# Performance work log

Hardware: AMD Instinct MI355X
Metric: run time of the kernel (lower is better)

## Reference

```python
import jax, jax.numpy as jnp
import numpy as np

B, D, C_IN = 2, 64, 4
N1, N2, N3, N4 = 32, 64, 96, 128
MQ, K = 1024, 5
DN = ('NCDHW', 'OIDHW', 'NCDHW')
PAD = [(2, 2)] * 3  # centered 5^3 kernel, matches Minkowski offsets in [-2, 2]


def setup_inputs() -> dict:
    rng = np.random.default_rng(0)
    mask = rng.random((B, D, D, D)) < 0.2
    x_feat = (rng.standard_normal((B, C_IN, D, D, D)) * mask[:, None]).astype(np.float32)
    Q_F = rng.random((B, MQ, 2)).astype(np.float32)  # per-point quality features (2 channels)

    def conv(cin, cout):
        w = (rng.standard_normal((cout, cin, K, K, K)) / np.sqrt(cin * K ** 3)).astype(np.float32)
        b = (0.01 * rng.standard_normal(cout)).astype(np.float32)
        return w, b

    def gdn(c):
        beta = np.ones(c, np.float32)
        gamma = (1e-4 * rng.random((c, c, K, K, K))).astype(np.float32)
        gamma[np.arange(c), np.arange(c), K // 2, K // 2, K // 2] += 0.1
        return beta, gamma

    w1, b1 = conv(C_IN, N1)
    w2, b2 = conv(N1, N2)
    w3, b3 = conv(N2, N3)
    w4, b4 = conv(N3, N4)
    beta1, gamma1 = gdn(N1)
    beta2, gamma2 = gdn(N2)
    beta3, gamma3 = gdn(N3)
    out = dict(x_feat=x_feat, mask=mask, Q_F=Q_F,
               w1=w1, b1=b1, w2=w2, b2=b2, w3=w3, b3=b3, w4=w4, b4=b4,
               beta1=beta1, gamma1=gamma1, beta2=beta2, gamma2=gamma2,
               beta3=beta3, gamma3=gamma3)
    return {k: jnp.asarray(v) for k, v in out.items()}


def _conv3d(x, w, b, stride):
    y = jax.lax.conv_general_dilated(x, w, (stride,) * 3, PAD, dimension_numbers=DN)
    return y + b[None, :, None, None, None]


def _pool_mask(m):
    # Minkowski stride-2 output coords = any occupied input in each 2x2x2 cell
    b, d = m.shape[0], m.shape[1]
    return m.reshape(b, d // 2, 2, d // 2, 2, d // 2, 2).max(axis=(2, 4, 6))


def _gdn(x, beta, gamma, scale, m):
    # conditional GDN: y = x / sqrt(beta + conv5(gamma, x^2)), scaled per batch by q[:,0]
    den = jax.lax.conv_general_dilated(x * x, gamma, (1, 1, 1), PAD, dimension_numbers=DN)
    y = x * jax.lax.rsqrt(beta[None, :, None, None, None] + den)
    return y * scale * m[:, None]


def reference(x_feat, mask, Q_F, w1, b1, w2, b2, w3, b3, w4, b4,
              beta1, gamma1, beta2, gamma2, beta3, gamma3):
    m0 = mask.astype(x_feat.dtype)
    q = jnp.mean(Q_F, axis=1)[None]                       # [1, B, 2]: per-batch mean of Q.F
    scale = q[0, :, 0][:, None, None, None, None]         # per-batch conditional scale

    c0 = m0.sum(axis=(1, 2, 3))                           # count_per_batch(x)
    m1 = _pool_mask(m0)
    x = _gdn(_conv3d(x_feat, w1, b1, 2) * m1[:, None], beta1, gamma1, scale, m1)
    c1 = m1.sum(axis=(1, 2, 3))
    m2 = _pool_mask(m1)
    x = _gdn(_conv3d(x, w2, b2, 2) * m2[:, None], beta2, gamma2, scale, m2)
    c2 = m2.sum(axis=(1, 2, 3))
    m3 = _pool_mask(m2)
    x = _gdn(_conv3d(x, w3, b3, 2) * m3[:, None], beta3, gamma3, scale, m3)
    x = _conv3d(x, w4, b4, 1) * m3[:, None]               # stride-1 conv keeps coords
    k = jnp.stack([c2, c1, c0]).astype(jnp.int32)         # k.reverse() in the original
    return x, q, k
```

## Files before the change

### kernel.cpp

```cpp
#include <hip/hip_runtime.h>
#include <math.h>

constexpr int Bn  = 2;
constexpr int CIN = 4;
constexpr int MQn = 1024;
constexpr int D0 = 64, D1 = 32, D2 = 16, D3 = 8;

constexpr int OUT_X = 0;
constexpr int OUT_Q = 131072;
constexpr int OUT_K = 131076;

constexpr size_t OFF_CNT   = 0;
constexpr size_t OFF_ZERO  = 8;
constexpr size_t OFF_D1    = 16;
constexpr size_t OFF_T2    = OFF_D1 + 2097152;
constexpr size_t OFF_D2    = OFF_T2 + 524288;
constexpr size_t OFF_T3    = OFF_D2 + 524288;
constexpr size_t OFF_D3    = OFF_T3 + 98304;
constexpr size_t ZERO_END  = OFF_D3 + 98304;
constexpr size_t OFF_SCALE = 3342360;
constexpr size_t OFF_M1    = 3342368;
constexpr size_t OFF_M2    = OFF_M1 + 65536;
constexpr size_t OFF_M3    = OFF_M2 + 8192;
constexpr size_t OFF_T1    = OFF_M3 + 1024;
constexpr size_t OFF_Y1    = OFF_T1 + 2097152;
constexpr size_t OFF_Y2    = OFF_Y1 + 2097152;
constexpr size_t OFF_SQ1   = OFF_Y2 + 524288;
constexpr size_t OFF_SQ2   = OFF_SQ1 + 1048576;
constexpr size_t OFF_SQ3   = OFF_SQ2 + 262144;
constexpr size_t OFF_Y3C   = OFF_SQ3 + 49152;
constexpr size_t OFF_W1T   = OFF_Y3C + 49152;
constexpr size_t OFF_W2T   = OFF_W1T + 16000;
constexpr size_t OFF_W3T   = OFF_W2T + 256000;
constexpr size_t OFF_WB1   = OFF_W3T + 768000;
constexpr size_t OFF_WB2   = OFF_WB1 + 64000;
constexpr size_t OFF_WB3   = OFF_WB2 + 256000;
constexpr size_t OFF_WB4   = OFF_WB3 + 576000;
constexpr size_t OFF_PU    = 12248736;
constexpr size_t OFF_Y1P   = OFF_PU + 9437184;
constexpr size_t OFF_WB2S  = OFF_Y1P + 3145728;
constexpr size_t OFF_WB1S  = OFF_WB2S + 384000;
constexpr size_t OFF_WB3S  = OFF_WB1S + 32000;
constexpr size_t OFF_Y2HL  = OFF_WB3S + 1152000;

typedef float v4f __attribute__((ext_vector_type(4)));
typedef __attribute__((ext_vector_type(8)))  short bf16x8v;
typedef __attribute__((ext_vector_type(4)))  short bf16x4v;
typedef __attribute__((ext_vector_type(16))) float f32x16v;

__device__ __forceinline__ void async_copy16(const float* g, float* l) {
    __builtin_amdgcn_global_load_lds(
        (const __attribute__((address_space(1))) void*)g,
        (__attribute__((address_space(3))) void*)l, 16, 0, 0);
}
__device__ __forceinline__ unsigned short f2bf(float f) {
    unsigned u = __float_as_uint(f);
    return (unsigned short)((u + 0x7FFFu + ((u >> 16) & 1u)) >> 16);
}
__device__ __forceinline__ float bf2f(unsigned short h) {
    return __uint_as_float((unsigned)h << 16);
}

__global__ void qmean_kernel(const float* __restrict__ QF, float* __restrict__ out_q,
                             float* __restrict__ scale) {
    int b = blockIdx.x >> 1, c = blockIdx.x & 1;
    float s = 0.f;
    for (int m = threadIdx.x; m < MQn; m += blockDim.x)
        s += QF[(b * MQn + m) * 2 + c];
    __shared__ float sh[256];
    sh[threadIdx.x] = s;
    __syncthreads();
    for (int st = 128; st > 0; st >>= 1) {
        if (threadIdx.x < st) sh[threadIdx.x] += sh[threadIdx.x + st];
        __syncthreads();
    }
    if (threadIdx.x == 0) {
        float mean = sh[0] / (float)MQn;
        out_q[b * 2 + c] = mean;
        if (c == 0) scale[b] = mean;
    }
}

__global__ void mask_pool1_kernel(const float* __restrict__ xf, float* __restrict__ m1,
                                  float* __restrict__ c0) {
    int idx = blockIdx.x * blockDim.x + threadIdx.x;
    int b = idx >> 15;
    int v = idx & 32767;
    int oz = v >> 10, oy = (v >> 5) & 31, ox = v & 31;
    float cnt = 0.f, mx = 0.f;
    for (int dz = 0; dz < 2; ++dz)
        for (int dy = 0; dy < 2; ++dy)
            for (int dx = 0; dx < 2; ++dx) {
                int z = 2 * oz + dz, y = 2 * oy + dy, x = 2 * ox + dx;
                size_t base = (size_t)b * CIN * D0 * D0 * D0 + ((size_t)z * D0 + y) * D0 + x;
                bool occ = false;
                for (int c = 0; c < CIN; ++c)
                    occ = occ || (xf[base + (size_t)c * D0 * D0 * D0] != 0.f);
                if (occ) { cnt += 1.f; mx = 1.f; }
            }
    m1[idx] = mx;
    __shared__ float sh[256];
    sh[threadIdx.x] = cnt;
    __syncthreads();
    for (int st = 128; st > 0; st >>= 1) {
        if (threadIdx.x < st) sh[threadIdx.x] += sh[threadIdx.x + st];
        __syncthreads();
    }
    if (threadIdx.x == 0) atomicAdd(&c0[b], sh[0]);
}

__global__ void pool_kernel(const float* __restrict__ min_, float* __restrict__ mout,
                            float* __restrict__ cacc, int Din) {
    int Do = Din >> 1;
    int per = Do * Do * Do;
    int idx = blockIdx.x * blockDim.x + threadIdx.x;
    int b = idx / per;
    int v = idx % per;
    int oz = v / (Do * Do), oy = (v / Do) % Do, ox = v % Do;
    float s = 0.f, mx = 0.f;
    for (int dz = 0; dz < 2; ++dz)
        for (int dy = 0; dy < 2; ++dy)
            for (int dx = 0; dx < 2; ++dx) {
                float val = min_[(((size_t)b * Din + 2 * oz + dz) * Din + 2 * oy + dy) * Din + 2 * ox + dx];
                s += val;
                mx = fmaxf(mx, val);
            }
    mout[idx] = mx;
    __shared__ float sh[256];
    sh[threadIdx.x] = s;
    __syncthreads();
    for (int st = 128; st > 0; st >>= 1) {
        if (threadIdx.x < st) sh[threadIdx.x] += sh[threadIdx.x + st];
        __syncthreads();
    }
    if (threadIdx.x == 0) atomicAdd(&cacc[b], sh[0]);
}

__global__ void writek_kernel(const float* __restrict__ cnt, float* __restrict__ outk) {
    int i = threadIdx.x;
    if (i < 6) {
        int row = i >> 1, b = i & 1;
        float v = (row == 0) ? cnt[4 + b] : (row == 1 ? cnt[2 + b] : cnt[b]);
        outk[i] = v;
    }
}

constexpr int MS1 = 0,        ME1 = 128000;
constexpr int MS2 = 128000,   ME2 = 640000;
constexpr int MS3 = 640000,   ME3 = 1792000;
constexpr int MS4 = 1792000,  ME4 = 3328000;
__global__ __launch_bounds__(256) void mwtrans_all_kernel(
        const float* __restrict__ g1, const float* __restrict__ g2,
        const float* __restrict__ g3, const float* __restrict__ w4,
        float* __restrict__ ws) {
    int idx = blockIdx.x * 256 + threadIdx.x;
    if (idx >= ME4) return;
    const float* src; unsigned short* dst; int nchn, cin, o;
    if (idx < ME1)      { src = g1; dst = (unsigned short*)(ws + OFF_WB1); nchn = 1; cin = 32; o = idx - MS1; }
    else if (idx < ME2) { src = g2; dst = (unsigned short*)(ws + OFF_WB2); nchn = 2; cin = 64; o = idx - MS2; }
    else if (idx < ME3) { src = g3; dst = (unsigned short*)(ws + OFF_WB3); nchn = 3; cin = 96; o = idx - MS3; }
    else                { src = w4; dst = (unsigned short*)(ws + OFF_WB4); nchn = 4; cin = 96; o = idx - MS4; }
    int j  = o & 7;
    int kc = (o >> 3) & 1;
    int n  = (o >> 4) & 31;
    int q  = o >> 9;
    int tap = q % 125;
    int q2  = q / 125;
    int nch = q2 % nchn;
    int cs  = q2 / nchn;
    int co = nch * 32 + n;
    int ci = cs * 16 + kc * 8 + j;
    dst[o] = f2bf(src[((size_t)co * cin + ci) * 125 + tap]);
}

constexpr int W2S_N = 768000;
__global__ __launch_bounds__(256) void w2s_kernel(const float* __restrict__ w2,
        unsigned short* __restrict__ dst) {
    int o = blockIdx.x * 256 + threadIdx.x;
    if (o >= W2S_N) return;
    int j = o & 7; int kc = (o >> 3) & 1; int n = (o >> 4) & 31; int q = o >> 9;
    int tap = q % 125; int q2 = q / 125; int c = q2 & 1; int cs = q2 >> 1;
    int co = c * 32 + n;
    int e = cs * 16 + kc * 8 + j;
    int ci = e & 31;
    float wv = w2[((size_t)co * 32 + ci) * 125 + tap];
    unsigned short h = f2bf(wv);
    if (e >= 64) h = f2bf(wv - bf2f(h));
    dst[o] = h;
}

constexpr int W3S_N = 2304000;
__global__ __launch_bounds__(256) void w3s_kernel(const float* __restrict__ w3,
        unsigned short* __restrict__ dst) {
    int o = blockIdx.x * 256 + threadIdx.x;
    if (o >= W3S_N) return;
    int j = o & 7; int kc = (o >> 3) & 1; int n = (o >> 4) & 31; int q = o >> 9;
    int tap = q % 125; int q2 = q / 125; int nch = q2 % 3; int cs = q2 / 3;
    int co = nch * 32 + n;
    int e = cs * 16 + kc * 8 + j;
    int ci = e & 63;
    float wv = w3[((size_t)co * 64 + ci) * 125 + tap];
    unsigned short h = f2bf(wv);
    if (e >= 128) h = f2bf(wv - bf2f(h));
    dst[o] = h;
}

constexpr int W1S_N = 64000;
__global__ __launch_bounds__(256) void w1s_kernel(const float* __restrict__ w1,
        unsigned short* __restrict__ dst) {
    int o = blockIdx.x * 256 + threadIdx.x;
    if (o >= W1S_N) return;
    int j = o & 7; int kc = (o >> 3) & 1; int n = (o >> 4) & 31; int tap = o >> 9;
    int ci = j & 3;
    unsigned short h;
    float wv = w1[((size_t)n * 4 + ci) * 125 + tap];
    unsigned short hi = f2bf(wv);
    if (kc == 0)       h = hi;
    else if (j < 4)    h = f2bf(wv - bf2f(hi));
    else               h = 0;
    dst[o] = h;
}

__global__ __launch_bounds__(256) void xcl_kernel(const float* __restrict__ xf,
        unsigned short* __restrict__ xcl) {
    int idx = blockIdx.x * 256 + threadIdx.x;
    int s = idx & 262143; int b = idx >> 18;
    bf16x8v o;
#pragma unroll
    for (int ci = 0; ci < 4; ++ci) {
        float f = xf[((size_t)(b * 4 + ci) << 18) + s];
        unsigned short h = f2bf(f);
        o[ci] = (short)h;
        o[4 + ci] = (short)f2bf(f - bf2f(h));
    }
    *(bf16x8v*)(xcl + (size_t)idx * 8) = o;
}

__global__ __launch_bounds__(256) void mconv1_s2_kernel(
    const unsigned short* __restrict__ xcl,
    const unsigned short* __restrict__ wb,
    const float* __restrict__ bias, const float* __restrict__ mask,
    const float* __restrict__ zerow,
    float* __restrict__ t1, unsigned short* __restrict__ sqcl)
{
    constexpr int DIN = 64, DOUT = 32;
    constexpr int NTX = 4, NTY = 8;
    int r = blockIdx.x;
    int tx0 = (r % NTX) * 8; r /= NTX;
    int ty0 = (r % NTY) * 4; r /= NTY;
    int tz0 = (r % 8) * 4;   int b = r / 8;

    int tid = threadIdx.x;
    int lane = tid & 63, w = tid >> 6;
    int n = lane & 31, kc = lane >> 5;
    int oz = tz0 + w, oy = ty0 + (n >> 3), ox = tx0 + (n & 7);

    f32x16v acc;
#pragma unroll
    for (int i = 0; i < 16; ++i) acc[i] = 0.f;

#pragma unroll 1
    for (int kz = 0; kz < 5; ++kz) {
        int gz = 2 * oz + kz - 2;
        bool zok = (unsigned)gz < (unsigned)DIN;
#pragma unroll 1
        for (int ky = 0; ky < 5; ++ky) {
            int gy = 2 * oy + ky - 2;
            bool zyok = zok && ((unsigned)gy < (unsigned)DIN);
            long long rowbase = (((long long)(b * DIN + gz) * DIN + gy) * DIN) * 8;
#pragma unroll
            for (int kx = 0; kx < 5; ++kx) {
                int gx = 2 * ox + kx - 2;
                bool ok = zyok && ((unsigned)gx < (unsigned)DIN);
                const unsigned short* g = ok ? xcl + (rowbase + (long long)gx * 8)
                                             : (const unsigned short*)zerow;
                bf16x8v dfrag = *(const bf16x8v*)g;
                int tap = (kz * 5 + ky) * 5 + kx;
                const unsigned short* wp = wb + ((size_t)tap << 9) + n * 16 + kc * 8;
                bf16x8v wfrag = *(const bf16x8v*)wp;
                acc = __builtin_amdgcn_mfma_f32_32x32x16_bf16(wfrag, dfrag, acc, 0, 0, 0);
            }
        }
    }

    int sp = (oz * DOUT + oy) * DOUT + ox;
    float mval = mask[b * DOUT * DOUT * DOUT + sp];
#pragma unroll
    for (int q = 0; q < 4; ++q) {
        int co0 = 8 * q + 4 * kc;
        bf16x4v s4;
#pragma unroll
        for (int j = 0; j < 4; ++j) {
            int co = co0 + j;
            float v = (acc[4 * q + j] + bias[co]) * mval;
            t1[(size_t)(b * 32 + co) * 32768 + sp] = v;
            s4[j] = (short)f2bf(v * v);
        }
        *(bf16x4v*)(sqcl + ((size_t)(b * 32768 + sp)) * 32 + co0) = s4;
    }
}

__global__ __launch_bounds__(128) void gdn_cl1_kernel(const float* __restrict__ t,
        const float* __restrict__ pd, const float* __restrict__ beta,
        const float* __restrict__ scale, unsigned short* __restrict__ y1p) {
    constexpr size_t NTOT = (size_t)Bn * 32 * 32768;
    constexpr size_t PLSZ = (size_t)Bn * 32768 * 16;
    int idx = blockIdx.x * 128 + threadIdx.x;
    int sp = idx & 32767; int b = idx >> 15;
    float sc = scale[b];
    bf16x8v hi[4], lo[4];
#pragma unroll
    for (int g = 0; g < 4; ++g) {
#pragma unroll
        for (int j = 0; j < 8; ++j) {
            int ci = g * 8 + j;
            size_t p = (size_t)(b * 32 + ci) * 32768 + sp;
            float den = pd[p] + pd[NTOT + p];
            float v = t[p] * rsqrtf(beta[ci] + den) * sc;
            unsigned short h = f2bf(v);
            hi[g][j] = (short)h;
            lo[g][j] = (short)f2bf(v - bf2f(h));
        }
    }
    size_t vo = ((size_t)b * 32768 + sp) * 16;
    *(bf16x8v*)(y1p + 0 * PLSZ + vo)     = hi[0];
    *(bf16x8v*)(y1p + 0 * PLSZ + vo + 8) = hi[1];
    *(bf16x8v*)(y1p + 1 * PLSZ + vo)     = hi[2];
    *(bf16x8v*)(y1p + 1 * PLSZ + vo + 8) = hi[3];
    *(bf16x8v*)(y1p + 2 * PLSZ + vo)     = lo[0];
    *(bf16x8v*)(y1p + 2 * PLSZ + vo + 8) = lo[1];
    *(bf16x8v*)(y1p + 3 * PLSZ + vo)     = lo[2];
    *(bf16x8v*)(y1p + 3 * PLSZ + vo + 8) = lo[3];
}

__global__ __launch_bounds__(128) void gdn_cl2_kernel(const float* __restrict__ t,
        const float* __restrict__ pd, const float* __restrict__ beta,
        const float* __restrict__ scale, unsigned short* __restrict__ yhl) {
    constexpr size_t NTOT = (size_t)Bn * 64 * 4096;
    int idx = blockIdx.x * 128 + threadIdx.x;
    if (idx >= Bn * 4096) return;
    int sp = idx & 4095; int b = idx >> 12;
    float sc = scale[b];
    bf16x8v blk[24];
#pragma unroll
    for (int g = 0; g < 8; ++g) {
#pragma unroll
        for (int j = 0; j < 8; ++j) {
            int ci = g * 8 + j;
            size_t p = (size_t)(b * 64 + ci) * 4096 + sp;
            float den = pd[p] + pd[NTOT + p] + pd[2 * NTOT + p] + pd[3 * NTOT + p];
            float v = t[p] * rsqrtf(beta[ci] + den) * sc;
            unsigned short h = f2bf(v);
            blk[g][j] = (short)h;
            blk[8 + g][j] = (short)f2bf(v - bf2f(h));
            blk[16 + g][j] = (short)h;
        }
    }
    unsigned short* o = yhl + (size_t)idx * 192;
#pragma unroll
    for (int g = 0; g < 24; ++g) *(bf16x8v*)(o + g * 8) = blk[g];
}

template<int COUTt, int DIN, int DOUT, int CIG, int ZSPL, int PLN>
__global__ __launch_bounds__(256) void mconv_s2p_kernel(
    const unsigned short* __restrict__ in,
    const unsigned short* __restrict__ wb,
    const float* __restrict__ zerow,
    float* __restrict__ pout)
{
    constexpr int NCH = COUTt / 32;
    constexpr int NTZ = DOUT / 4, NTY = DOUT / 4, NTX = (DOUT >= 8) ? DOUT / 8 : 1;
    constexpr int NT = NTZ * NTY * NTX * Bn;
    constexpr int VOX = DOUT * DOUT * DOUT;
    constexpr size_t PLSZ = (size_t)Bn * DIN * DIN * DIN * 16;

    int tile = blockIdx.x % NT; int rest = blockIdx.x / NT;
    int cs = rest % CIG; int zig = rest / CIG;
    int pl = cs % PLN;
    int r = tile;
    int tx0 = (r % NTX) * 8; r /= NTX;
    int ty0 = (r % NTY) * 4; r /= NTY;
    int tz0 = (r % NTZ) * 4; int b = r / NTZ;

    int tid = threadIdx.x;
    int lane = tid & 63, w = tid >> 6;
    int n = lane & 31, kc = lane >> 5;
    int oz = tz0 + w, oy = ty0 + (n >> 3), ox = tx0 + (n & 7);

    const unsigned short* inp = in + (size_t)pl * PLSZ;

    f32x16v acc[NCH];
#pragma unroll
    for (int c = 0; c < NCH; ++c)
#pragma unroll
        for (int i = 0; i < 16; ++i) acc[c][i] = 0.f;

    int kzlo, kzhi;
    if (ZSPL == 5)      { kzlo = zig;     kzhi = zig + 1; }
    else if (ZSPL == 3) { kzlo = 2 * zig; kzhi = (2 * zig + 2 < 5) ? 2 * zig + 2 : 5; }
    else                { kzlo = 0;       kzhi = 5; }
#pragma unroll 1
    for (int kz = kzlo; kz < kzhi; ++kz) {
        int gz = 2 * oz + kz - 2;
        bool zok = (unsigned)gz < (unsigned)DIN;
#pragma unroll 1
        for (int ky = 0; ky < 5; ++ky) {
            int gy = 2 * oy + ky - 2;
            bool zyok = zok && ((unsigned)gy < (unsigned)DIN);
            long long rowbase = (((long long)(b * DIN + gz) * DIN + gy) * DIN) * 16 + kc * 8;
#pragma unroll
            for (int kx = 0; kx < 5; ++kx) {
                int gx = 2 * ox + kx - 2;
                bool ok = zyok && ((unsigned)gx < (unsigned)DIN);
                const unsigned short* g = ok ? inp + (rowbase + (long long)gx * 16)
                                             : (const unsigned short*)zerow;
                bf16x8v dfrag = *(const bf16x8v*)g;
                int tap = (kz * 5 + ky) * 5 + kx;
#pragma unroll
                for (int c = 0; c < NCH; ++c) {
                    const unsigned short* wp =
                        wb + (((size_t)(cs * NCH + c) * 125 + tap) << 9) + n * 16 + kc * 8;
                    bf16x8v wfrag = *(const bf16x8v*)wp;
                    acc[c] = __builtin_amdgcn_mfma_f32_32x32x16_bf16(wfrag, dfrag, acc[c], 0, 0, 0);
                }
            }
        }
    }

    int sp = (oz * DOUT + oy) * DOUT + ox;
#pragma unroll
    for (int c = 0; c < NCH; ++c) {
#pragma unroll
        for (int rr = 0; rr < 16; ++rr) {
            int co = c * 32 + (rr & 3) + 8 * (rr >> 2) + 4 * kc;
            pout[((size_t)((zig * CIG + cs) * Bn + b) * COUTt + co) * VOX + sp] = acc[c][rr];
        }
    }
}

template<int CINe, int COUTt, int DIN, int DOUT, int CIG, int ZSPL>
__global__ __launch_bounds__(256) void mconv_s2_kernel(
    const unsigned short* __restrict__ in,
    const unsigned short* __restrict__ wb,
    const float* __restrict__ zerow,
    float* __restrict__ pout)
{
    constexpr int NCH = COUTt / 32;
    constexpr int NTZ = DOUT / 4, NTY = DOUT / 4, NTX = (DOUT >= 8) ? DOUT / 8 : 1;
    constexpr int NT = NTZ * NTY * NTX * Bn;
    constexpr int VOX = DOUT * DOUT * DOUT;

    int tile = blockIdx.x % NT; int rest = blockIdx.x / NT;
    int cs = rest % CIG; int zig = rest / CIG;
    int r = tile;
    int tx0 = (r % NTX) * 8; r /= NTX;
    int ty0 = (r % NTY) * 4; r /= NTY;
    int tz0 = (r % NTZ) * 4; int b = r / NTZ;

    int tid = threadIdx.x;
    int lane = tid & 63, w = tid >> 6;
    int n = lane & 31, kc = lane >> 5;
    int oz = tz0 + w, oy = ty0 + (n >> 3), ox = tx0 + (n & 7);

    f32x16v acc[NCH];
#pragma unroll
    for (int c = 0; c < NCH; ++c)
#pragma unroll
        for (int i = 0; i < 16; ++i) acc[c][i] = 0.f;

    int kzlo, kzhi;
    if (ZSPL == 5)      { kzlo = zig;     kzhi = zig + 1; }
    else if (ZSPL == 3) { kzlo = 2 * zig; kzhi = (2 * zig + 2 < 5) ? 2 * zig + 2 : 5; }
    else                { kzlo = 0;       kzhi = 5; }
#pragma unroll 1
    for (int kz = kzlo; kz < kzhi; ++kz) {
        int gz = 2 * oz + kz - 2;
        bool zok = (unsigned)gz < (unsigned)DIN;
#pragma unroll 1
        for (int ky = 0; ky < 5; ++ky) {
            int gy = 2 * oy + ky - 2;
            bool zyok = zok && ((unsigned)gy < (unsigned)DIN);
            long long rowbase = (((long long)(b * DIN + gz) * DIN + gy) * DIN) * CINe
                                + cs * 16 + kc * 8;
#pragma unroll
            for (int kx = 0; kx < 5; ++kx) {
                int gx = 2 * ox + kx - 2;
                bool ok = zyok && ((unsigned)gx < (unsigned)DIN);
                const unsigned short* g = ok ? in + (rowbase + (long long)gx * CINe)
                                             : (const unsigned short*)zerow;
                bf16x8v dfrag = *(const bf16x8v*)g;
                int tap = (kz * 5 + ky) * 5 + kx;
#pragma unroll
                for (int c = 0; c < NCH; ++c) {
                    const unsigned short* wp =
                        wb + (((size_t)(cs * NCH + c) * 125 + tap) << 9) + n * 16 + kc * 8;
                    bf16x8v wfrag = *(const bf16x8v*)wp;
                    acc[c] = __builtin_amdgcn_mfma_f32_32x32x16_bf16(wfrag, dfrag, acc[c], 0, 0, 0);
                }
            }
        }
    }

    int sp = (oz * DOUT + oy) * DOUT + ox;
#pragma unroll
    for (int c = 0; c < NCH; ++c) {
#pragma unroll
        for (int rr = 0; rr < 16; ++rr) {
            int co = c * 32 + (rr & 3) + 8 * (rr >> 2) + 4 * kc;
            pout[((size_t)((zig * CIG + cs) * Bn + b) * COUTt + co) * VOX + sp] = acc[c][rr];
        }
    }
}

template<int CS, int COUTt, int VOX>
__global__ __launch_bounds__(256) void red_epi_kernel(const float* __restrict__ P,
        const float* __restrict__ bias, const float* __restrict__ mask,
        float* __restrict__ buf, unsigned short* __restrict__ sqcl) {
    constexpr int NTOT = Bn * COUTt * VOX;
    int idx = blockIdx.x * 256 + threadIdx.x;
    if (idx >= NTOT) return;
    int sp = idx % VOX;
    int co = (idx / VOX) % COUTt;
    int b = idx / (VOX * COUTt);
    float s = 0.f;
#pragma unroll
    for (int k = 0; k < CS; ++k) s += P[(size_t)k * NTOT + idx];
    float v = (s + bias[co]) * mask[b * VOX + sp];
    buf[idx] = v;
    sqcl[((size_t)b * VOX + sp) * COUTt + co] = f2bf(v * v);
}

template<int CINt, int COUTt, int Dd, int TZ, int YB, int CIG, int ZSPL>
__global__ __launch_bounds__(256) void mconv_kernel(
    const unsigned short* __restrict__ in,
    const unsigned short* __restrict__ wb,
    const float* __restrict__ zerow,
    float* __restrict__ pout)
{
    constexpr int NCH = COUTt / 32;
    constexpr int LZ = TZ + 4, LYH = YB * 4 + 4, LXH = 12;
    constexpr int HV = LZ * LYH * LXH;
    constexpr int UN = 2 * HV;
    constexpr int NLOAD = (UN + 255) / 256;
    constexpr int NTZ = Dd / TZ, NTY = Dd / (YB * 4), NTX = Dd / 8;
    constexpr int NT = NTZ * NTY * NTX * Bn;
    constexpr int VOX = Dd * Dd * Dd;
    __shared__ unsigned short lds[NLOAD * 256 * 8];

    int bid = blockIdx.x;
    int tile = bid % NT; int rest = bid / NT;
    int cs = rest % CIG; int zig = rest / CIG;
    int r = tile;
    int tx0 = (r % NTX) * 8; r /= NTX;
    int ty0 = (r % NTY) * (YB * 4); r /= NTY;
    int tz0 = (r % NTZ) * TZ; int b = r / NTZ;

    int tid = threadIdx.x;
    int iz0 = tz0 - 2, iy0 = ty0 - 2, ix0 = tx0 - 2;
#pragma unroll
    for (int k = 0; k < NLOAD; ++k) {
        int u = tid + k * 256;
        int v = u >> 1, half = u & 1;
        int lx = v % LXH; int t = v / LXH;
        int ly = t % LYH, lz = t / LYH;
        int gz = iz0 + lz, gy = iy0 + ly, gx = ix0 + lx;
        bool valid = (v < HV) &&
                     (unsigned)gz < (unsigned)Dd && (unsigned)gy < (unsigned)Dd &&
                     (unsigned)gx < (unsigned)Dd;
        const unsigned short* g = valid
            ? in + ((((size_t)b * Dd + gz) * Dd + gy) * Dd + gx) * CINt + cs * 16 + half * 8
            : (const unsigned short*)zerow;
        async_copy16((const float*)g, (float*)&lds[(size_t)u * 8]);
    }
    __syncthreads();

    int lane = tid & 63, w = tid >> 6;
    int zz = (YB == 1) ? w : (w >> 1);
    int yb = (YB == 1) ? 0 : (w & 1);
    int n = lane & 31, kc = lane >> 5;
    int vy = yb * 4 + (n >> 3), vx = n & 7;

    f32x16v acc[NCH];
#pragma unroll
    for (int c = 0; c < NCH; ++c)
#pragma unroll
        for (int i = 0; i < 16; ++i) acc[c][i] = 0.f;

    int kzlo = (ZSPL == 5) ? zig : 0;
    int kzhi = (ZSPL == 5) ? zig + 1 : 5;
#pragma unroll 1
    for (int kz = kzlo; kz < kzhi; ++kz) {
#pragma unroll 1
        for (int ky = 0; ky < 5; ++ky) {
            int hvrow = ((zz + kz) * LYH + (vy + ky)) * LXH + vx;
#pragma unroll
            for (int kx = 0; kx < 5; ++kx) {
                bf16x8v dfrag = *(const bf16x8v*)&lds[(size_t)(hvrow + kx) * 16 + kc * 8];
                int tap = (kz * 5 + ky) * 5 + kx;
#pragma unroll
                for (int c = 0; c < NCH; ++c) {
                    const unsigned short* wp =
                        wb + (((size_t)(cs * NCH + c) * 125 + tap) << 9) + n * 16 + kc * 8;
                    bf16x8v wfrag = *(const bf16x8v*)wp;
                    acc[c] = __builtin_amdgcn_mfma_f32_32x32x16_bf16(wfrag, dfrag, acc[c], 0, 0, 0);
                }
            }
        }
    }

    int g = rest;
    int sp = ((tz0 + zz) * Dd + (ty0 + vy)) * Dd + (tx0 + vx);
#pragma unroll
    for (int c = 0; c < NCH; ++c) {
#pragma unroll
        for (int rr = 0; rr < 16; ++rr) {
            int co = c * 32 + (rr & 3) + 8 * (rr >> 2) + 4 * kc;
            pout[((size_t)(g * Bn + b) * COUTt + co) * VOX + sp] = acc[c][rr];
        }
    }
}

template<int G, int COUTt, int DOUT>
__global__ __launch_bounds__(256) void gdn_red_cl_kernel(const float* __restrict__ t,
        const float* __restrict__ pd, const float* __restrict__ beta,
        const float* __restrict__ scale, unsigned short* __restrict__ ycl) {
    constexpr int VOX = DOUT * DOUT * DOUT;
    constexpr int NTOT = Bn * COUTt * VOX;
    int idx = blockIdx.x * 256 + threadIdx.x;
    if (idx >= NTOT) return;
    int sp = idx % VOX;
    int co = (idx / VOX) % COUTt;
    int b = idx / (VOX * COUTt);
    float den = 0.f;
#pragma unroll
    for (int k = 0; k < G; ++k) den += pd[(size_t)k * NTOT + idx];
    float v = t[idx] * rsqrtf(beta[co] + den) * scale[b];
    ycl[((size_t)b * VOX + sp) * COUTt + co] = f2bf(v);
}

template<int G, int COUTt, int DOUT>
__global__ __launch_bounds__(256) void conv_red_kernel(const float* __restrict__ pc,
        const float* __restrict__ bias, const float* __restrict__ mask,
        float* __restrict__ outx) {
    constexpr int VOX = DOUT * DOUT * DOUT;
    constexpr int NTOT = Bn * COUTt * VOX;
    int idx = blockIdx.x * 256 + threadIdx.x;
    if (idx >= NTOT) return;
    int sp = idx % VOX;
    int co = (idx / VOX) % COUTt;
    int b = idx / (VOX * COUTt);
    float s = 0.f;
#pragma unroll
    for (int k = 0; k < G; ++k) s += pc[(size_t)k * NTOT + idx];
    outx[idx] = (s + bias[co]) * mask[b * VOX + sp];
}

extern "C" void kernel_launch(void* const* d_in, const int* in_sizes, int n_in,
                              void* d_out, int out_size, void* d_ws, size_t ws_size,
                              hipStream_t stream) {
    const float* x_feat = (const float*)d_in[0];
    const float* QF     = (const float*)d_in[2];
    const float* w1 = (const float*)d_in[3];  const float* b1 = (const float*)d_in[4];
    const float* w2 = (const float*)d_in[5];  const float* b2 = (const float*)d_in[6];
    const float* w3 = (const float*)d_in[7];  const float* b3 = (const float*)d_in[8];
    const float* w4 = (const float*)d_in[9];  const float* b4 = (const float*)d_in[10];
    const float* beta1 = (const float*)d_in[11]; const float* gamma1 = (const float*)d_in[12];
    const float* beta2 = (const float*)d_in[13]; const float* gamma2 = (const float*)d_in[14];
    const float* beta3 = (const float*)d_in[15]; const float* gamma3 = (const float*)d_in[16];

    float* out = (float*)d_out;
    float* ws = (float*)d_ws;
    float* cnt   = ws + OFF_CNT;
    float* zerow = ws + OFF_ZERO;
    float* scale = ws + OFF_SCALE;
    float* m1 = ws + OFF_M1;  float* m2 = ws + OFF_M2;  float* m3 = ws + OFF_M3;
    float* t1 = ws + OFF_T1;
    float* t2 = ws + OFF_T2;
    float* t3 = ws + OFF_T3;
    float* pu = ws + OFF_PU;
    unsigned short* sq1 = (unsigned short*)(ws + OFF_SQ1);
    unsigned short* sq2 = (unsigned short*)(ws + OFF_SQ2);
    unsigned short* sq3 = (unsigned short*)(ws + OFF_SQ3);
    unsigned short* y3c = (unsigned short*)(ws + OFF_Y3C);
    unsigned short* y1p = (unsigned short*)(ws + OFF_Y1P);
    unsigned short* y2hl = (unsigned short*)(ws + OFF_Y2HL);
    unsigned short* xcl = (unsigned short*)(ws + OFF_Y1);
    unsigned short* wb1 = (unsigned short*)(ws + OFF_WB1);
    unsigned short* wb2 = (unsigned short*)(ws + OFF_WB2);
    unsigned short* wb3 = (unsigned short*)(ws + OFF_WB3);
    unsigned short* wb4 = (unsigned short*)(ws + OFF_WB4);
    unsigned short* wb1s = (unsigned short*)(ws + OFF_WB1S);
    unsigned short* wb2s = (unsigned short*)(ws + OFF_WB2S);
    unsigned short* wb3s = (unsigned short*)(ws + OFF_WB3S);

    hipMemsetAsync(ws, 0, 16 * sizeof(float), stream);

    qmean_kernel<<<4, 256, 0, stream>>>(QF, out + OUT_Q, scale);
    mask_pool1_kernel<<<256, 256, 0, stream>>>(x_feat, m1, cnt + 0);
    pool_kernel<<<32, 256, 0, stream>>>(m1, m2, cnt + 2, D1);
    pool_kernel<<<4, 256, 0, stream>>>(m2, m3, cnt + 4, D2);
    writek_kernel<<<1, 64, 0, stream>>>(cnt, out + OUT_K);

    mwtrans_all_kernel<<<(ME4 + 255) / 256, 256, 0, stream>>>(gamma1, gamma2, gamma3, w4, ws);
    w1s_kernel<<<(W1S_N + 255) / 256, 256, 0, stream>>>(w1, wb1s);
    w2s_kernel<<<(W2S_N + 255) / 256, 256, 0, stream>>>(w2, wb2s);
    w3s_kernel<<<(W3S_N + 255) / 256, 256, 0, stream>>>(w3, wb3s);
    xcl_kernel<<<2048, 256, 0, stream>>>(x_feat, xcl);

    mconv1_s2_kernel<<<512, 256, 0, stream>>>(xcl, wb1s, b1, m1, zerow, t1, sq1);
    mconv_kernel<32, 32, 32, 4, 1, 2, 1>
        <<<1024, 256, 0, stream>>>(sq1, wb1, zerow, pu);
    gdn_cl1_kernel<<<512, 128, 0, stream>>>(t1, pu, beta1, scale, y1p);

    mconv_s2p_kernel<64, 32, 16, 6, 3, 4>
        <<<64 * 6 * 3, 256, 0, stream>>>(y1p, wb2s, zerow, pu);
    red_epi_kernel<18, 64, 4096><<<2048, 256, 0, stream>>>(pu, b2, m2, t2, sq2);
    mconv_kernel<64, 64, 16, 4, 1, 4, 1>
        <<<256, 256, 0, stream>>>(sq2, wb2, zerow, pu);
    gdn_cl2_kernel<<<64, 128, 0, stream>>>(t2, pu, beta2, scale, y2hl);

    mconv_s2_kernel<192, 96, 16, 8, 12, 5>
        <<<8 * 12 * 5, 256, 0, stream>>>(y2hl, wb3s, zerow, pu);
    red_epi_kernel<60, 96, 512><<<384, 256, 0, stream>>>(pu, b3, m3, t3, sq3);
    mconv_kernel<96, 96, 8, 2, 2, 6, 5>
        <<<240, 256, 0, stream>>>(sq3, wb3, zerow, pu);
    gdn_red_cl_kernel<30, 96, 8><<<384, 256, 0, stream>>>(t3, pu, beta3, scale, y3c);

    mconv_kernel<96, 128, 8, 2, 2, 6, 5>
        <<<240, 256, 0, stream>>>(y3c, wb4, zerow, pu);
    conv_red_kernel<30, 128, 8><<<512, 256, 0, stream>>>(pu, b4, m3, out + OUT_X);
}
```

Baseline: 399.6 us.

## Fuse prep kernels and run GDN1 conv without channel-split partials

Merges the layer-1 mask pooling with the bf16 hi/lo channels-last conversion of the input. The two coarser pool passes become one kernel, and the four weight-transform kernels become a single launch. The mconv kernel gains an inner loop over several 16-channel slices per block, so the GDN1 conv can run with CIG=1: one partial buffer and half the blocks, with no two-partial sum in gdn_cl1. This removes launch overhead and the split-reduction traffic, but gives fewer blocks for the first GDN conv and a larger LDS tile per block.

New measurement: 409.0 us. 2.3% more time.

```diff
diff --git a/kernel.cpp b/kernel.cpp
--- a/kernel.cpp
+++ b/kernel.cpp
@@ -81,9 +81,10 @@
     }
 }
 
-__global__ void mask_pool1_kernel(const float* __restrict__ xf, float* __restrict__ m1,
-                                  float* __restrict__ c0) {
-    int idx = blockIdx.x * blockDim.x + threadIdx.x;
+__global__ __launch_bounds__(256) void maskxcl_kernel(const float* __restrict__ xf,
+        float* __restrict__ m1, float* __restrict__ c0,
+        unsigned short* __restrict__ xcl) {
+    int idx = blockIdx.x * 256 + threadIdx.x;
     int b = idx >> 15;
     int v = idx & 32767;
     int oz = v >> 10, oy = (v >> 5) & 31, ox = v & 31;
@@ -92,10 +93,19 @@
         for (int dy = 0; dy < 2; ++dy)
             for (int dx = 0; dx < 2; ++dx) {
                 int z = 2 * oz + dz, y = 2 * oy + dy, x = 2 * ox + dx;
-                size_t base = (size_t)b * CIN * D0 * D0 * D0 + ((size_t)z * D0 + y) * D0 + x;
+                size_t s = ((size_t)z * D0 + y) * D0 + x;
+                size_t base = (size_t)b * CIN * 262144 + s;
                 bool occ = false;
-                for (int c = 0; c < CIN; ++c)
-                    occ = occ || (xf[base + (size_t)c * D0 * D0 * D0] != 0.f);
+                bf16x8v o;
+#pragma unroll
+                for (int c = 0; c < 4; ++c) {
+                    float f = xf[base + (size_t)c * 262144];
+                    occ = occ || (f != 0.f);
+                    unsigned short h = f2bf(f);
+                    o[c] = (short)h;
+                    o[4 + c] = (short)f2bf(f - bf2f(h));
+                }
+                *(bf16x8v*)(xcl + ((size_t)b * 262144 + s) * 8) = o;
                 if (occ) { cnt += 1.f; mx = 1.f; }
             }
     m1[idx] = mx;
@@ -109,31 +119,52 @@
     if (threadIdx.x == 0) atomicAdd(&c0[b], sh[0]);
 }
 
-__global__ void pool_kernel(const float* __restrict__ min_, float* __restrict__ mout,
-                            float* __restrict__ cacc, int Din) {
-    int Do = Din >> 1;
-    int per = Do * Do * Do;
-    int idx = blockIdx.x * blockDim.x + threadIdx.x;
-    int b = idx / per;
-    int v = idx % per;
-    int oz = v / (Do * Do), oy = (v / Do) % Do, ox = v % Do;
-    float s = 0.f, mx = 0.f;
-    for (int dz = 0; dz < 2; ++dz)
-        for (int dy = 0; dy < 2; ++dy)
-            for (int dx = 0; dx < 2; ++dx) {
-                float val = min_[(((size_t)b * Din + 2 * oz + dz) * Din + 2 * oy + dy) * Din + 2 * ox + dx];
-                s += val;
-                mx = fmaxf(mx, val);
+__global__ __launch_bounds__(256) void pool23_kernel(const float* __restrict__ m1,
+        float* __restrict__ m2, float* __restrict__ m3, float* __restrict__ cnt) {
+    int idx = blockIdx.x * 256 + threadIdx.x;
+    int b = idx >> 9;
+    int v = idx & 511;
+    int oz = v >> 6, oy = (v >> 3) & 7, ox = v & 7;
+    float s1 = 0.f, s2 = 0.f, mx3 = 0.f;
+#pragma unroll
+    for (int a = 0; a < 2; ++a)
+#pragma unroll
+        for (int bb = 0; bb < 2; ++bb)
+#pragma unroll
+            for (int cc = 0; cc < 2; ++cc) {
+                float mx2 = 0.f;
+#pragma unroll
+                for (int dz = 0; dz < 2; ++dz)
+#pragma unroll
+                    for (int dy = 0; dy < 2; ++dy)
+#pragma unroll
+                        for (int dx = 0; dx < 2; ++dx) {
+                            int z = 4 * oz + 2 * a + dz, y = 4 * oy + 2 * bb + dy,
+                                x = 4 * ox + 2 * cc + dx;
+                            float val = m1[(((size_t)b * 32 + z) * 32 + y) * 32 + x];
+                            s1 += val;
+                            mx2 = fmaxf(mx2, val);
+                        }
+                m2[(((size_t)b * 16 + 2 * oz + a) * 16 + 2 * oy + bb) * 16 + 2 * ox + cc] = mx2;
+                s2 += mx2;
+                mx3 = fmaxf(mx3, mx2);
             }
-    mout[idx] = mx;
-    __shared__ float sh[256];
-    sh[threadIdx.x] = s;
+    m3[idx] = mx3;
+    __shared__ float sh[256][2];
+    sh[threadIdx.x][0] = s1;
+    sh[threadIdx.x][1] = s2;
     __syncthreads();
     for (int st = 128; st > 0; st >>= 1) {
-        if (threadIdx.x < st) sh[threadIdx.x] += sh[threadIdx.x + st];
+        if (threadIdx.x < st) {
+            sh[threadIdx.x][0] += sh[threadIdx.x + st][0];
+            sh[threadIdx.x][1] += sh[threadIdx.x + st][1];
+        }
         __syncthreads();
     }
-    if (threadIdx.x == 0) atomicAdd(&cacc[b], sh[0]);
+    if (threadIdx.x == 0) {
+        atomicAdd(&cnt[2 + b], sh[0][0]);
+        atomicAdd(&cnt[4 + b], sh[0][1]);
+    }
 }
 
 __global__ void writek_kernel(const float* __restrict__ cnt, float* __restrict__ outk) {
@@ -149,91 +180,70 @@
 constexpr int MS2 = 128000,   ME2 = 640000;
 constexpr int MS3 = 640000,   ME3 = 1792000;
 constexpr int MS4 = 1792000,  ME4 = 3328000;
-__global__ __launch_bounds__(256) void mwtrans_all_kernel(
+constexpr int W1S_N = 64000;
+constexpr int W2S_N = 768000;
+constexpr int W3S_N = 2304000;
+constexpr int WALL2 = ME4 + W1S_N;
+constexpr int WALL3 = WALL2 + W2S_N;
+constexpr int WALL_N = WALL3 + W3S_N;
+__global__ __launch_bounds__(256) void wall_kernel(
         const float* __restrict__ g1, const float* __restrict__ g2,
         const float* __restrict__ g3, const float* __restrict__ w4,
-        float* __restrict__ ws) {
+        const float* __restrict__ w1, const float* __restrict__ w2,
+        const float* __restrict__ w3, float* __restrict__ ws) {
     int idx = blockIdx.x * 256 + threadIdx.x;
-    if (idx >= ME4) return;
-    const float* src; unsigned short* dst; int nchn, cin, o;
-    if (idx < ME1)      { src = g1; dst = (unsigned short*)(ws + OFF_WB1); nchn = 1; cin = 32; o = idx - MS1; }
-    else if (idx < ME2) { src = g2; dst = (unsigned short*)(ws + OFF_WB2); nchn = 2; cin = 64; o = idx - MS2; }
-    else if (idx < ME3) { src = g3; dst = (unsigned short*)(ws + OFF_WB3); nchn = 3; cin = 96; o = idx - MS3; }
-    else                { src = w4; dst = (unsigned short*)(ws + OFF_WB4); nchn = 4; cin = 96; o = idx - MS4; }
-    int j  = o & 7;
-    int kc = (o >> 3) & 1;
-    int n  = (o >> 4) & 31;
-    int q  = o >> 9;
-    int tap = q % 125;
-    int q2  = q / 125;
-    int nch = q2 % nchn;
-    int cs  = q2 / nchn;
-    int co = nch * 32 + n;
-    int ci = cs * 16 + kc * 8 + j;
-    dst[o] = f2bf(src[((size_t)co * cin + ci) * 125 + tap]);
-}
-
-constexpr int W2S_N = 768000;
-__global__ __launch_bounds__(256) void w2s_kernel(const float* __restrict__ w2,
-        unsigned short* __restrict__ dst) {
-    int o = blockIdx.x * 256 + threadIdx.x;
-    if (o >= W2S_N) return;
-    int j = o & 7; int kc = (o >> 3) & 1; int n = (o >> 4) & 31; int q = o >> 9;
-    int tap = q % 125; int q2 = q / 125; int c = q2 & 1; int cs = q2 >> 1;
-    int co = c * 32 + n;
-    int e = cs * 16 + kc * 8 + j;
-    int ci = e & 31;
-    float wv = w2[((size_t)co * 32 + ci) * 125 + tap];
-    unsigned short h = f2bf(wv);
-    if (e >= 64) h = f2bf(wv - bf2f(h));
-    dst[o] = h;
-}
-
-constexpr int W3S_N = 2304000;
-__global__ __launch_bounds__(256) void w3s_kernel(const float* __restrict__ w3,
-        unsigned short* __restrict__ dst) {
-    int o = blockIdx.x * 256 + threadIdx.x;
-    if (o >= W3S_N) return;
-    int j = o & 7; int kc = (o >> 3) & 1; int n = (o >> 4) & 31; int q = o >> 9;
-    int tap = q % 125; int q2 = q / 125; int nch = q2 % 3; int cs = q2 / 3;
-    int co = nch * 32 + n;
-    int e = cs * 16 + kc * 8 + j;
-    int ci = e & 63;
-    float wv = w3[((size_t)co * 64 + ci) * 125 + tap];
-    unsigned short h = f2bf(wv);
-    if (e >= 128) h = f2bf(wv - bf2f(h));
-    dst[o] = h;
-}
-
-constexpr int W1S_N = 64000;
-__global__ __launch_bounds__(256) void w1s_kernel(const float* __restrict__ w1,
-        unsigned short* __restrict__ dst) {
-    int o = blockIdx.x * 256 + threadIdx.x;
-    if (o >= W1S_N) return;
-    int j = o & 7; int kc = (o >> 3) & 1; int n = (o >> 4) & 31; int tap = o >> 9;
-    int ci = j & 3;
-    unsigned short h;
-    float wv = w1[((size_t)n * 4 + ci) * 125 + tap];
-    unsigned short hi = f2bf(wv);
-    if (kc == 0)       h = hi;
-    else if (j < 4)    h = f2bf(wv - bf2f(hi));
-    else               h = 0;
-    dst[o] = h;
-}
-
-__global__ __launch_bounds__(256) void xcl_kernel(const float* __restrict__ xf,
-        unsigned short* __restrict__ xcl) {
-    int idx = blockIdx.x * 256 + threadIdx.x;
-    int s = idx & 262143; int b = idx >> 18;
-    bf16x8v o;
-#pragma unroll
-    for (int ci = 0; ci < 4; ++ci) {
-        float f = xf[((size_t)(b * 4 + ci) << 18) + s];
-        unsigned short h = f2bf(f);
-        o[ci] = (short)h;
-        o[4 + ci] = (short)f2bf(f - bf2f(h));
-    }
-    *(bf16x8v*)(xcl + (size_t)idx * 8) = o;
+    if (idx >= WALL_N) return;
+    if (idx < ME4) {
+        const float* src; unsigned short* dst; int nchn, cin, o;
+        if (idx < ME1)      { src = g1; dst = (unsigned short*)(ws + OFF_WB1); nchn = 1; cin = 32; o = idx - MS1; }
+        else if (idx < ME2) { src = g2; dst = (unsigned short*)(ws + OFF_WB2); nchn = 2; cin = 64; o = idx - MS2; }
+        else if (idx < ME3) { src = g3; dst = (unsigned short*)(ws + OFF_WB3); nchn = 3; cin = 96; o = idx - MS3; }
+        else                { src = w4; dst = (unsigned short*)(ws + OFF_WB4); nchn = 4; cin = 96; o = idx - MS4; }
+        int j  = o & 7;
+        int kc = (o >> 3) & 1;
+        int n  = (o >> 4) & 31;
+        int q  = o >> 9;
+        int tap = q % 125;
+        int q2  = q / 125;
+        int nch = q2 % nchn;
+        int cs  = q2 / nchn;
+        int co = nch * 32 + n;
+        int ci = cs * 16 + kc * 8 + j;
+        dst[o] = f2bf(src[((size_t)co * cin + ci) * 125 + tap]);
+    } else if (idx < WALL2) {
+        int o = idx - ME4;
+        int j = o & 7; int kc = (o >> 3) & 1; int n = (o >> 4) & 31; int tap = o >> 9;
+        int ci = j & 3;
+        unsigned short h;
+        float wv = w1[((size_t)n * 4 + ci) * 125 + tap];
+        unsigned short hi = f2bf(wv);
+        if (kc == 0)       h = hi;
+        else if (j < 4)    h = f2bf(wv - bf2f(hi));
+        else               h = 0;
+        ((unsigned short*)(ws + OFF_WB1S))[o] = h;
+    } else if (idx < WALL3) {
+        int o = idx - WALL2;
+        int j = o & 7; int kc = (o >> 3) & 1; int n = (o >> 4) & 31; int q = o >> 9;
+        int tap = q % 125; int q2 = q / 125; int c = q2 & 1; int cs = q2 >> 1;
+        int co = c * 32 + n;
+        int e = cs * 16 + kc * 8 + j;
+        int ci = e & 31;
+        float wv = w2[((size_t)co * 32 + ci) * 125 + tap];
+        unsigned short h = f2bf(wv);
+        if (e >= 64) h = f2bf(wv - bf2f(h));
+        ((unsigned short*)(ws + OFF_WB2S))[o] = h;
+    } else {
+        int o = idx - WALL3;
+        int j = o & 7; int kc = (o >> 3) & 1; int n = (o >> 4) & 31; int q = o >> 9;
+        int tap = q % 125; int q2 = q / 125; int nch = q2 % 3; int cs = q2 / 3;
+        int co = nch * 32 + n;
+        int e = cs * 16 + kc * 8 + j;
+        int ci = e & 63;
+        float wv = w3[((size_t)co * 64 + ci) * 125 + tap];
+        unsigned short h = f2bf(wv);
+        if (e >= 128) h = f2bf(wv - bf2f(h));
+        ((unsigned short*)(ws + OFF_WB3S))[o] = h;
+    }
 }
 
 __global__ __launch_bounds__(256) void mconv1_s2_kernel(
@@ -303,7 +313,6 @@
 __global__ __launch_bounds__(128) void gdn_cl1_kernel(const float* __restrict__ t,
         const float* __restrict__ pd, const float* __restrict__ beta,
         const float* __restrict__ scale, unsigned short* __restrict__ y1p) {
-    constexpr size_t NTOT = (size_t)Bn * 32 * 32768;
     constexpr size_t PLSZ = (size_t)Bn * 32768 * 16;
     int idx = blockIdx.x * 128 + threadIdx.x;
     int sp = idx & 32767; int b = idx >> 15;
@@ -315,7 +324,7 @@
         for (int j = 0; j < 8; ++j) {
             int ci = g * 8 + j;
             size_t p = (size_t)(b * 32 + ci) * 32768 + sp;
-            float den = pd[p] + pd[NTOT + p];
+            float den = pd[p];
             float v = t[p] * rsqrtf(beta[ci] + den) * sc;
             unsigned short h = f2bf(v);
             hi[g][j] = (short)h;
@@ -538,9 +547,12 @@
     float* __restrict__ pout)
 {
     constexpr int NCH = COUTt / 32;
+    constexpr int CSPB = (CINt / 16) / CIG;
+    constexpr int UPV = 2 * CSPB;
+    constexpr int CHS = CSPB * 16;
     constexpr int LZ = TZ + 4, LYH = YB * 4 + 4, LXH = 12;
     constexpr int HV = LZ * LYH * LXH;
-    constexpr int UN = 2 * HV;
+    constexpr int UN = UPV * HV;
     constexpr int NLOAD = (UN + 255) / 256;
     constexpr int NTZ = Dd / TZ, NTY = Dd / (YB * 4), NTX = Dd / 8;
     constexpr int NT = NTZ * NTY * NTX * Bn;
@@ -560,7 +572,7 @@
 #pragma unroll
     for (int k = 0; k < NLOAD; ++k) {
         int u = tid + k * 256;
-        int v = u >> 1, half = u & 1;
+        int v = u / UPV, part = u % UPV;
         int lx = v % LXH; int t = v / LXH;
         int ly = t % LYH, lz = t / LYH;
         int gz = iz0 + lz, gy = iy0 + ly, gx = ix0 + lx;
@@ -568,7 +580,7 @@
                      (unsigned)gz < (unsigned)Dd && (unsigned)gy < (unsigned)Dd &&
                      (unsigned)gx < (unsigned)Dd;
         const unsigned short* g = valid
-            ? in + ((((size_t)b * Dd + gz) * Dd + gy) * Dd + gx) * CINt + cs * 16 + half * 8
+            ? in + ((((size_t)b * Dd + gz) * Dd + gy) * Dd + gx) * CINt + cs * CHS + part * 8
             : (const unsigned short*)zerow;
         async_copy16((const float*)g, (float*)&lds[(size_t)u * 8]);
     }
@@ -589,20 +601,25 @@
     int kzlo = (ZSPL == 5) ? zig : 0;
     int kzhi = (ZSPL == 5) ? zig + 1 : 5;
 #pragma unroll 1
-    for (int kz = kzlo; kz < kzhi; ++kz) {
-#pragma unroll 1
-        for (int ky = 0; ky < 5; ++ky) {
-            int hvrow = ((zz + kz) * LYH + (vy + ky)) * LXH + vx;
-#pragma unroll
-            for (int kx = 0; kx < 5; ++kx) {
-                bf16x8v dfrag = *(const bf16x8v*)&lds[(size_t)(hvrow + kx) * 16 + kc * 8];
-                int tap = (kz * 5 + ky) * 5 + kx;
-#pragma unroll
-                for (int c = 0; c < NCH; ++c) {
-                    const unsigned short* wp =
-                        wb + (((size_t)(cs * NCH + c) * 125 + tap) << 9) + n * 16 + kc * 8;
-                    bf16x8v wfrag = *(const bf16x8v*)wp;
-                    acc[c] = __builtin_amdgcn_mfma_f32_32x32x16_bf16(wfrag, dfrag, acc[c], 0, 0, 0);
+    for (int csl = 0; csl < CSPB; ++csl) {
+        int csabs = cs * CSPB + csl;
+#pragma unroll 1
+        for (int kz = kzlo; kz < kzhi; ++kz) {
+#pragma unroll 1
+            for (int ky = 0; ky < 5; ++ky) {
+                int hvrow = ((zz + kz) * LYH + (vy + ky)) * LXH + vx;
+#pragma unroll
+                for (int kx = 0; kx < 5; ++kx) {
+                    bf16x8v dfrag =
+                        *(const bf16x8v*)&lds[(size_t)(hvrow + kx) * CHS + csl * 16 + kc * 8];
+                    int tap = (kz * 5 + ky) * 5 + kx;
+#pragma unroll
+                    for (int c = 0; c < NCH; ++c) {
+                        const unsigned short* wp =
+                            wb + (((size_t)(csabs * NCH + c) * 125 + tap) << 9) + n * 16 + kc * 8;
+                        bf16x8v wfrag = *(const bf16x8v*)wp;
+                        acc[c] = __builtin_amdgcn_mfma_f32_32x32x16_bf16(wfrag, dfrag, acc[c], 0, 0, 0);
+                    }
                 }
             }
         }
@@ -696,20 +713,16 @@
     hipMemsetAsync(ws, 0, 16 * sizeof(float), stream);
 
     qmean_kernel<<<4, 256, 0, stream>>>(QF, out + OUT_Q, scale);
-    mask_pool1_kernel<<<256, 256, 0, stream>>>(x_feat, m1, cnt + 0);
-    pool_kernel<<<32, 256, 0, stream>>>(m1, m2, cnt + 2, D1);
-    pool_kernel<<<4, 256, 0, stream>>>(m2, m3, cnt + 4, D2);
+    maskxcl_kernel<<<256, 256, 0, stream>>>(x_feat, m1, cnt + 0, xcl);
+    pool23_kernel<<<4, 256, 0, stream>>>(m1, m2, m3, cnt);
     writek_kernel<<<1, 64, 0, stream>>>(cnt, out + OUT_K);
 
-    mwtrans_all_kernel<<<(ME4 + 255) / 256, 256, 0, stream>>>(gamma1, gamma2, gamma3, w4, ws);
-    w1s_kernel<<<(W1S_N + 255) / 256, 256, 0, stream>>>(w1, wb1s);
-    w2s_kernel<<<(W2S_N + 255) / 256, 256, 0, stream>>>(w2, wb2s);
-    w3s_kernel<<<(W3S_N + 255) / 256, 256, 0, stream>>>(w3, wb3s);
-    xcl_kernel<<<2048, 256, 0, stream>>>(x_feat, xcl);
+    wall_kernel<<<(WALL_N + 255) / 256, 256, 0, stream>>>(
+        gamma1, gamma2, gamma3, w4, w1, w2, w3, ws);
 
     mconv1_s2_kernel<<<512, 256, 0, stream>>>(xcl, wb1s, b1, m1, zerow, t1, sq1);
-    mconv_kernel<32, 32, 32, 4, 1, 2, 1>
-        <<<1024, 256, 0, stream>>>(sq1, wb1, zerow, pu);
+    mconv_kernel<32, 32, 32, 4, 1, 1, 1>
+        <<<512, 256, 0, stream>>>(sq1, wb1, zerow, pu);
     gdn_cl1_kernel<<<512, 128, 0, stream>>>(t1, pu, beta1, scale, y1p);
 
     mconv_s2p_kernel<64, 32, 16, 6, 3, 4>
```
